# Optimization experiments

Hardware: AMD Instinct MI355X
Metric: run time of the kernel (lower is better)

## Reference

```python
import jax, jax.numpy as jnp
import numpy as np
from jax import lax

D_MODEL, D_STATE, D_CONV, D_INNER, DT_RANK = 1024, 16, 4, 2048, 64
B_SZ, L_SEQ = 2, 4096

def setup_inputs() -> dict:
    key = jax.random.key(0)
    ks = jax.random.split(key, 12)
    s = 0.02
    x = jax.random.normal(ks[0], (B_SZ, L_SEQ, D_MODEL), jnp.float32)
    norm_w = jnp.ones((D_MODEL,), jnp.float32)
    norm_b = jnp.zeros((D_MODEL,), jnp.float32)
    W_in = jax.random.normal(ks[1], (D_MODEL, 2 * D_INNER), jnp.float32) * s
    conv_w = jax.random.normal(ks[2], (D_INNER, 1, D_CONV), jnp.float32) * 0.5
    conv_b = jnp.zeros((D_INNER,), jnp.float32)
    W_x = jax.random.normal(ks[3], (D_INNER, DT_RANK + 2 * D_STATE), jnp.float32) * s
    W_dt = jax.random.normal(ks[4], (DT_RANK, D_INNER), jnp.float32) * s
    # dt bias init as in the torch module: inverse-softplus of dt in [dt_min, dt_max]
    dt_init = jnp.exp(jax.random.uniform(ks[5], (D_INNER,)) * (np.log(0.1) - np.log(0.001)) + np.log(0.001))
    dt_init = jnp.clip(dt_init, 1e-4, None)
    b_dt = dt_init + jnp.log(-jnp.expm1(-dt_init))
    A_log = jnp.log(jnp.broadcast_to(jnp.arange(1, D_STATE + 1, dtype=jnp.float32)[None, :], (D_INNER, D_STATE)))
    D = jnp.ones((D_INNER,), jnp.float32)
    W_out = jax.random.normal(ks[6], (D_INNER, D_MODEL), jnp.float32) * s
    return {"x": x, "norm_w": norm_w, "norm_b": norm_b, "W_in": W_in,
            "conv_w": conv_w, "conv_b": conv_b, "W_x": W_x, "W_dt": W_dt,
            "b_dt": b_dt, "A_log": A_log, "D": D, "W_out": W_out}

def _silu(v):
    return v * jax.nn.sigmoid(v)

def _layernorm(v, w, b, eps=1e-5):
    mu = jnp.mean(v, axis=-1, keepdims=True)
    var = jnp.var(v, axis=-1, keepdims=True)
    return (v - mu) * lax.rsqrt(var + eps) * w + b

def _selective_scan(u, delta, A, Bm, Cm, Dp):
    # u, delta: [B,L,d_inner]; A: [d_inner,N]; Bm, Cm: [B,L,N]; Dp: [d_inner]
    Bb, L, d_inner = u.shape
    N = A.shape[1]

    def step(h, inp):
        dt_t, u_t, B_t, C_t = inp  # [B,d_inner],[B,d_inner],[B,N],[B,N]
        A_bar = jnp.exp(dt_t[..., None] * A)                       # [B,d_inner,N]
        h = A_bar * h + dt_t[..., None] * B_t[:, None, :] * u_t[..., None]
        y = jnp.sum(h * C_t[:, None, :], axis=-1)                  # [B,d_inner]
        return h, y

    h0 = jnp.zeros((Bb, d_inner, N), u.dtype)
    xs = (jnp.swapaxes(delta, 0, 1), jnp.swapaxes(u, 0, 1),
          jnp.swapaxes(Bm, 0, 1), jnp.swapaxes(Cm, 0, 1))
    _, ys = lax.scan(step, h0, xs)          # ys: [L,B,d_inner]
    y = jnp.swapaxes(ys, 0, 1)
    return y + u * Dp[None, None, :]

def reference(x, norm_w, norm_b, W_in, conv_w, conv_b, W_x, W_dt, b_dt, A_log, D, W_out):
    residual = x
    xn = _layernorm(x, norm_w, norm_b)
    xz = xn @ W_in                                      # [B,L,2*d_inner]
    x_ssm, z = jnp.split(xz, 2, axis=-1)
    # depthwise causal conv1d (torch pads both sides then truncates -> left pad)
    xt = jnp.swapaxes(x_ssm, 1, 2)                      # [B,d_inner,L]
    xt = jnp.pad(xt, ((0, 0), (0, 0), (D_CONV - 1, 0)))
    xc = lax.conv_general_dilated(xt, conv_w, window_strides=(1,), padding='VALID',
                                  feature_group_count=D_INNER,
                                  dimension_numbers=('NCH', 'OIH', 'NCH'))
    xc = xc + conv_b[None, :, None]
    x_conv = jnp.swapaxes(_silu(xc), 1, 2)              # [B,L,d_inner]
    x_dbl = x_conv @ W_x                                # [B,L,dt_rank+2N]
    dt_low, B_mat, C_mat = jnp.split(x_dbl, [DT_RANK, DT_RANK + D_STATE], axis=-1)
    delta = jax.nn.softplus(dt_low @ W_dt + b_dt)       # [B,L,d_inner]
    A = -jnp.exp(A_log)
    y = _selective_scan(x_conv, delta, A, B_mat, C_mat, D)
    y = y * _silu(z)
    return residual + y @ W_out
```

## Files before the change

kernel.cpp:

```cpp
#include <hip/hip_runtime.h>

typedef unsigned short u16;
typedef __attribute__((ext_vector_type(8))) __bf16 bf16x8;
typedef __attribute__((ext_vector_type(4))) float f32x4;

#define LSEQ 4096
#define DMODEL 1024
#define DINNER 2048

__device__ __forceinline__ float bf2f(u16 u) {
  union { unsigned u; float f; } v; v.u = ((unsigned)u) << 16; return v.f;
}
__device__ __forceinline__ u16 f2bf(float f) {
  union { float f; unsigned u; } v; v.f = f;
  unsigned r = v.u + 0x7fffu + ((v.u >> 16) & 1u);
  return (u16)(r >> 16);
}
__device__ __forceinline__ void gload_lds16(const void* g, void* l) {
  __builtin_amdgcn_global_load_lds(
      (__attribute__((address_space(1))) void*)(unsigned long long)g,
      (__attribute__((address_space(3))) void*)(unsigned int)(unsigned long long)l,
      16, 0, 0);
}
__device__ __forceinline__ float sigmoidf_(float v) { return 1.f / (1.f + __expf(-v)); }

__device__ __forceinline__ void swz_block(int gx, int& bn, int& bm) {
  int lin = blockIdx.x + gridDim.x * blockIdx.y;
  int q = (gridDim.x * gridDim.y) >> 3;
  int s = (lin & 7) * q + (lin >> 3);
  bn = s % gx;
  bm = s / gx;
}

#define SBAR { __builtin_amdgcn_s_barrier(); __builtin_amdgcn_sched_barrier(0); }

__global__ __launch_bounds__(256) void tc_ln_all(const float* __restrict__ W_in,
                                                 const float* __restrict__ W_x,
                                                 const float* __restrict__ W_dt,
                                                 const float* __restrict__ W_out,
                                                 u16* __restrict__ o0, u16* __restrict__ o1,
                                                 u16* __restrict__ o2, u16* __restrict__ o3,
                                                 const float* __restrict__ x,
                                                 const float* __restrict__ nw,
                                                 const float* __restrict__ nb,
                                                 u16* __restrict__ xn_out) {
  int id = blockIdx.x;
  int t = threadIdx.x;
  if (id >= 6528) {
    int row = id - 6528;
    const float* xr = x + (size_t)row * DMODEL;
    float4 v = ((const float4*)xr)[t];
    float s = v.x + v.y + v.z + v.w;
    float s2 = v.x * v.x + v.y * v.y + v.z * v.z + v.w * v.w;
    for (int off = 32; off; off >>= 1) {
      s += __shfl_down(s, off);
      s2 += __shfl_down(s2, off);
    }
    __shared__ float ls[4], ls2[4];
    int wid = t >> 6;
    if ((t & 63) == 0) { ls[wid] = s; ls2[wid] = s2; }
    __syncthreads();
    s = ls[0] + ls[1] + ls[2] + ls[3];
    s2 = ls2[0] + ls2[1] + ls2[2] + ls2[3];
    float mu = s * (1.f / DMODEL);
    float var = s2 * (1.f / DMODEL) - mu * mu;
    float rs = rsqrtf(var + 1e-5f);
    float4 wv = ((const float4*)nw)[t];
    float4 bv = ((const float4*)nb)[t];
    unsigned p0 = (unsigned)f2bf((v.x - mu) * rs * wv.x + bv.x) |
                  ((unsigned)f2bf((v.y - mu) * rs * wv.y + bv.y) << 16);
    unsigned p1 = (unsigned)f2bf((v.z - mu) * rs * wv.z + bv.z) |
                  ((unsigned)f2bf((v.w - mu) * rs * wv.w + bv.w) << 16);
    ((uint2*)(xn_out + (size_t)row * DMODEL))[t] = make_uint2(p0, p1);
    return;
  }
  __shared__ float tile[32][33];
  const float* in;
  u16* out;
  int K, N, Npad, gx, bx;
  if (id < 4096)      { in = W_in;  out = o0; K = 1024; N = 4096; Npad = 4096; gx = 128; bx = id; }
  else if (id < 4352) { in = W_x;   out = o1; K = 2048; N = 96;   Npad = 128;  gx = 4;   bx = id - 4096; }
  else if (id < 4480) { in = W_dt;  out = o2; K = 64;   N = 2048; Npad = 2048; gx = 64;  bx = id - 4352; }
  else                { in = W_out; out = o3; K = 2048; N = 1024; Npad = 1024; gx = 32;  bx = id - 4480; }
  int n0 = (bx % gx) * 32, k0 = (bx / gx) * 32;
  int tx = t & 31, ty = t >> 5;
  for (int i = ty; i < 32; i += 8) {
    int k = k0 + i, n = n0 + tx;
    tile[i][tx] = (k < K && n < N) ? in[(size_t)k * N + n] : 0.f;
  }
  __syncthreads();
  for (int i = ty; i < 32; i += 8) {
    int n = n0 + i, k = k0 + tx;
    if (n < Npad && k < K) out[(size_t)n * K + k] = f2bf(tile[tx][i]);
  }
}

__device__ __forceinline__ void stage8(const u16* grow0, int ld, int kcol0,
                                       u16* lds_u, int ln) {
  int rr = ln >> 3, kb = ln & 7;
  gload_lds16(grow0 + (size_t)rr * ld + kcol0 + ((kb ^ rr) << 3), lds_u);
}

#define LDA_F(mh, BUF)                                                             \
  _Pragma("unroll") for (int mf = 0; mf < 4; ++mf) {                               \
    av[mf][0] = *(const bf16x8*)(qA0 + (BUF) * 16384 + ((mh) * 64 + mf * 16) * 64); \
    av[mf][1] = *(const bf16x8*)(qA1 + (BUF) * 16384 + ((mh) * 64 + mf * 16) * 64); \
  }

#define LDB_F(nh, BUF)                                                             \
  _Pragma("unroll") for (int nf = 0; nf < 2; ++nf) {                               \
    bb[nh][nf][0] = *(const bf16x8*)(qB0 + (BUF) * 16384 + ((nh) * 32 + nf * 16) * 64); \
    bb[nh][nf][1] = *(const bf16x8*)(qB1 + (BUF) * 16384 + ((nh) * 32 + nf * 16) * 64); \
  }

#define MFMA_Q(mh, nh)                                                             \
  __builtin_amdgcn_s_setprio(1);                                                   \
  _Pragma("unroll") for (int mf = 0; mf < 4; ++mf)                                 \
  _Pragma("unroll") for (int nf = 0; nf < 2; ++nf)                                 \
  _Pragma("unroll") for (int kk = 0; kk < 2; ++kk)                                 \
    acc[(mh) * 4 + mf][(nh) * 2 + nf] = __builtin_amdgcn_mfma_f32_16x16x32_bf16(   \
        av[mf][kk], bb[nh][nf][kk], acc[(mh) * 4 + mf][(nh) * 2 + nf], 0, 0, 0);   \
  __builtin_amdgcn_s_setprio(0);

#define STAGE_A(unit, kt, buf)                                                     \
  _Pragma("unroll") for (int c = 0; c < 2; ++c) {                                  \
    int g = w * 2 + c;                                                             \
    int r0 = ((g < 8) ? g * 8 : (g - 8) * 8 + 128) + (unit) * 64;                  \
    stage8(Ag + (size_t)r0 * ldK, ldK, (kt) * 64, LA + (buf) * 16384 + r0 * 64, ln); \
  }

#define STAGE_B(half, kt, buf)                                                     \
  _Pragma("unroll") for (int c = 0; c < 2; ++c) {                                  \
    int g = w * 2 + c;                                                             \
    int r0 = (g >> 2) * 64 + (half) * 32 + (g & 3) * 8;                            \
    stage8(Bg + (size_t)r0 * ldK, ldK, (kt) * 64, LB + (buf) * 16384 + r0 * 64, ln); \
  }

#define PHASES8P(T_, B0_, B1_)                                                     \
  {                                                                                \
    int kt1 = ((T_) + 1 < NT) ? (T_) + 1 : NT - 1;                                 \
    int kt2 = ((T_) + 2 < NT) ? (T_) + 2 : NT - 1;                                 \
    LDA_F(0, B0_); LDB_F(0, B0_); LDB_F(1, B0_);                                   \
    STAGE_A(1, kt1, B1_);                                                          \
    MFMA_Q(0, 0);                                                                  \
    MFMA_Q(0, 1);                                                                  \
    SBAR                                                                           \
    LDA_F(1, B0_);                                                                 \
    STAGE_A(0, kt2, B0_);                                                          \
    STAGE_B(0, kt2, B0_);                                                          \
    STAGE_B(1, kt2, B0_);                                                          \
    asm volatile("s_waitcnt vmcnt(6)" ::: "memory");                               \
    MFMA_Q(1, 1);                                                                  \
    MFMA_Q(1, 0);                                                                  \
    SBAR                                                                           \
  }

template <int OUT_BF16, int EPI>
__global__ __launch_bounds__(512, 2) void gemm8p(const u16* __restrict__ A,
                                                 const u16* __restrict__ Bt,
                                                 void* __restrict__ Cout,
                                                 const float* __restrict__ aux,
                                                 int M, int N, int K, int cthresh) {
  __shared__ alignas(16) u16 lds[65536];
  u16* LA = lds;
  u16* LB = lds + 32768;
  int t = threadIdx.x;
  int w = t >> 6, ln = t & 63;
  int wm = w >> 2, wn = w & 3;
  int bn, bm;
  swz_block(gridDim.x, bn, bm);
  int lr = ln & 15, lq = ln >> 4, key = ln & 7;
  int ldK = K;
  int NT = K >> 6;
  const u16* Ag = A + (size_t)bm * 256 * ldK;
  const u16* Bg = Bt + (size_t)bn * 256 * ldK;
  const u16* qA0 = LA + (wm * 128 + lr) * 64 + ((lq ^ key) << 3);
  const u16* qA1 = LA + (wm * 128 + lr) * 64 + (((4 + lq) ^ key) << 3);
  const u16* qB0 = LB + (wn * 64 + lr) * 64 + ((lq ^ key) << 3);
  const u16* qB1 = LB + (wn * 64 + lr) * 64 + (((4 + lq) ^ key) << 3);
  f32x4 acc[8][4] = {};
  bf16x8 av[4][2], bb[2][2][2];

  STAGE_A(0, 0, 0); STAGE_B(0, 0, 0); STAGE_B(1, 0, 0); STAGE_A(1, 0, 0);
  int k1 = NT > 1 ? 1 : 0;
  STAGE_A(0, k1, 1); STAGE_B(0, k1, 1); STAGE_B(1, k1, 1);
  asm volatile("s_waitcnt vmcnt(6)" ::: "memory");
  SBAR

  for (int TT = 0; TT < NT; TT += 2) {
    PHASES8P(TT, 0, 1)
    PHASES8P(TT + 1, 1, 0)
  }

  int crow0 = bm * 256 + wm * 128;
  int ccol0 = bn * 256 + wn * 64;
#pragma unroll
  for (int mf = 0; mf < 8; ++mf)
#pragma unroll
    for (int nf = 0; nf < 4; ++nf)
#pragma unroll
      for (int r = 0; r < 4; ++r) {
        int row = crow0 + mf * 16 + lq * 4 + r;
        int col = ccol0 + nf * 16 + lr;
        float v = acc[mf][nf][r];
        if (EPI == 1) v += aux[(size_t)row * N + col];
        if (EPI == 2 && col >= cthresh) v = v * sigmoidf_(v);
        if (OUT_BF16)
          ((u16*)Cout)[(size_t)row * N + col] = f2bf(v);
        else
          ((float*)Cout)[(size_t)row * N + col] = v;
      }
}

#define LDA128(mh, BUF)                                                            \
  _Pragma("unroll") for (int mf2 = 0; mf2 < 2; ++mf2) {                            \
    av[mf2][0] = *(const bf16x8*)(rA0 + (BUF) * 8192 + ((mh) * 32 + mf2 * 16) * 64); \
    av[mf2][1] = *(const bf16x8*)(rA1 + (BUF) * 8192 + ((mh) * 32 + mf2 * 16) * 64); \
  }

#define LDB128(nh, BUF, B_)                                                        \
  _Pragma("unroll") for (int nf2 = 0; nf2 < 2; ++nf2) {                            \
    B_[nf2][0] = *(const bf16x8*)(rB0 + (BUF) * 16384 + ((nh) * 32 + nf2 * 16) * 64); \
    B_[nf2][1] = *(const bf16x8*)(rB1 + (BUF) * 16384 + ((nh) * 32 + nf2 * 16) * 64); \
  }

#define MFMA_Q128(mh, nh, B_)                                                      \
  __builtin_amdgcn_s_setprio(1);                                                   \
  _Pragma("unroll") for (int mf2 = 0; mf2 < 2; ++mf2)                              \
  _Pragma("unroll") for (int nf2 = 0; nf2 < 2; ++nf2)                              \
  _Pragma("unroll") for (int kk = 0; kk < 2; ++kk)                                 \
    acc[(mh) * 2 + mf2][(nh) * 2 + nf2] = __builtin_amdgcn_mfma_f32_16x16x32_bf16( \
        av[mf2][kk], B_[nf2][kk], acc[(mh) * 2 + mf2][(nh) * 2 + nf2], 0, 0, 0);   \
  __builtin_amdgcn_s_setprio(0);

#define STAGE_A128(unit, kt, buf)                                                  \
  {                                                                                \
    int r0 = (w >> 2) * 64 + (unit) * 32 + (w & 3) * 8;                            \
    stage8(Ag + (size_t)r0 * ldK, ldK, (kt) * 64, LA + (buf) * 8192 + r0 * 64, ln); \
  }

#define STAGE_B128(half, kt, buf)                                                  \
  _Pragma("unroll") for (int c = 0; c < 2; ++c) {                                  \
    int g = w * 2 + c;                                                             \
    int r0 = (g >> 2) * 64 + (half) * 32 + (g & 3) * 8;                            \
    stage8(Bg + (size_t)r0 * ldK, ldK, (kt) * 64, LB + (buf) * 16384 + r0 * 64, ln); \
  }

#define PHASES128(T_, B0_, B1_)                                                    \
  {                                                                                \
    int kt1 = ((T_) + 1 < NT) ? (T_) + 1 : NT - 1;                                 \
    int kt2 = ((T_) + 2 < NT) ? (T_) + 2 : NT - 1;                                 \
    LDA128(0, B0_);                                                                \
    LDB128(0, B0_, bbl);                                                           \
    LDB128(1, B0_, bbh);                                                           \
    STAGE_A128(1, kt1, B1_);                                                       \
    MFMA_Q128(0, 0, bbl);                                                          \
    MFMA_Q128(0, 1, bbh);                                                          \
    SBAR                                                                           \
    LDA128(1, B0_);                                                                \
    STAGE_A128(0, kt2, B0_);                                                       \
    STAGE_B128(0, kt2, B0_);                                                       \
    STAGE_B128(1, kt2, B0_);                                                       \
    asm volatile("s_waitcnt vmcnt(5)" ::: "memory");                               \
    MFMA_Q128(1, 1, bbh);                                                          \
    MFMA_Q128(1, 0, bbl);                                                          \
    SBAR                                                                           \
  }

__global__ __launch_bounds__(512, 2) void gemm128_res(const u16* __restrict__ A,
                                                      const u16* __restrict__ Bt,
                                                      float* __restrict__ Cout,
                                                      const float* __restrict__ res,
                                                      int M, int N, int K) {
  __shared__ alignas(16) u16 lds[49152];
  u16* LA = lds;
  u16* LB = lds + 16384;
  int t = threadIdx.x;
  int w = t >> 6, ln = t & 63;
  int wm = w >> 2, wn = w & 3;
  int bn, bm;
  swz_block(gridDim.x, bn, bm);
  int lr = ln & 15, lq = ln >> 4, key = ln & 7;
  int ldK = K;
  int NT = K >> 6;
  const u16* Ag = A + (size_t)bm * 128 * ldK;
  const u16* Bg = Bt + (size_t)bn * 256 * ldK;
  const u16* rA0 = LA + (wm * 64 + lr) * 64 + ((lq ^ key) << 3);
  const u16* rA1 = LA + (wm * 64 + lr) * 64 + (((4 + lq) ^ key) << 3);
  const u16* rB0 = LB + (wn * 64 + lr) * 64 + ((lq ^ key) << 3);
  const u16* rB1 = LB + (wn * 64 + lr) * 64 + (((4 + lq) ^ key) << 3);
  f32x4 acc[4][4] = {};
  bf16x8 av[2][2], bbl[2][2], bbh[2][2];

  STAGE_A128(0, 0, 0); STAGE_B128(0, 0, 0); STAGE_B128(1, 0, 0); STAGE_A128(1, 0, 0);
  int k1 = NT > 1 ? 1 : 0;
  STAGE_A128(0, k1, 1); STAGE_B128(0, k1, 1); STAGE_B128(1, k1, 1);
  asm volatile("s_waitcnt vmcnt(5)" ::: "memory");
  SBAR

  for (int TT = 0; TT < NT; TT += 2) {
    PHASES128(TT, 0, 1)
    PHASES128(TT + 1, 1, 0)
  }

  int crow0 = bm * 128 + wm * 64;
  int ccol0 = bn * 256 + wn * 64;
#pragma unroll
  for (int mf = 0; mf < 4; ++mf)
#pragma unroll
    for (int nf = 0; nf < 4; ++nf)
#pragma unroll
      for (int r = 0; r < 4; ++r) {
        int row = crow0 + mf * 16 + lq * 4 + r;
        int col = ccol0 + nf * 16 + lr;
        Cout[(size_t)row * N + col] = acc[mf][nf][r] + res[(size_t)row * N + col];
      }
}

template <int OUT_BF16, int EPI, int SPLITK>
__global__ __launch_bounds__(256) void gemm_bt(const u16* __restrict__ A,
                                               const u16* __restrict__ Bt,
                                               void* __restrict__ Cout,
                                               const float* __restrict__ aux,
                                               int M, int N, int K, int ld, int cthresh) {
  __shared__ alignas(16) u16 As[128 * 32];
  __shared__ alignas(16) u16 Bs[128 * 32];
  int t = threadIdx.x;
  int w = t >> 6, ln = t & 63;
  int wr = w >> 1, wc = w & 1;
  int bm = blockIdx.y, bn = blockIdx.x;
  int lr = ln & 15, lk = (ln >> 4) * 8;
  f32x4 acc[4][4] = {};
  int kz = SPLITK ? blockIdx.z * K : 0;
  const u16* Abase = A + (size_t)bm * 128 * ld + kz;
  const u16* Bbase = Bt + (size_t)bn * 128 * ld + kz;
  for (int k0 = 0; k0 < K; k0 += 32) {
#pragma unroll
    for (int c = 0; c < 2; ++c) {
      int chunk = w * 2 + c;
      int ee = chunk * 512 + ln * 8;
      int row = ee >> 5, col = ee & 31;
      gload_lds16(Abase + (size_t)row * ld + k0 + col, As + chunk * 512);
      gload_lds16(Bbase + (size_t)row * ld + k0 + col, Bs + chunk * 512);
    }
    __syncthreads();
    bf16x8 af[4], bfr[4];
#pragma unroll
    for (int m = 0; m < 4; ++m)
      af[m] = *(const bf16x8*)(As + (wr * 64 + m * 16 + lr) * 32 + lk);
#pragma unroll
    for (int n = 0; n < 4; ++n)
      bfr[n] = *(const bf16x8*)(Bs + (wc * 64 + n * 16 + lr) * 32 + lk);
#pragma unroll
    for (int m = 0; m < 4; ++m)
#pragma unroll
      for (int n = 0; n < 4; ++n)
        acc[m][n] = __builtin_amdgcn_mfma_f32_16x16x32_bf16(af[m], bfr[n], acc[m][n], 0, 0, 0);
    __syncthreads();
  }
  int rb = bm * 128 + wr * 64 + (ln >> 4) * 4;
  int cb = bn * 128 + wc * 64 + lr;
  float* Cpart = SPLITK ? ((float*)Cout + (size_t)blockIdx.z * M * N) : (float*)Cout;
#pragma unroll
  for (int m = 0; m < 4; ++m)
#pragma unroll
    for (int n = 0; n < 4; ++n)
#pragma unroll
      for (int r = 0; r < 4; ++r) {
        int row = rb + m * 16 + r;
        int col = cb + n * 16;
        float v = acc[m][n][r];
        if (EPI == 3) {
          float dtr = v + aux[col];
          v = dtr > 15.f ? dtr : __logf(1.f + __expf(dtr));
        }
        if (OUT_BF16)
          ((u16*)Cpart)[(size_t)row * N + col] = f2bf(v);
        else
          Cpart[(size_t)row * N + col] = v;
      }
}

__global__ __launch_bounds__(256) void reduce_xdbl(const float* __restrict__ part,
                                                   float* __restrict__ xdbl,
                                                   u16* __restrict__ dtlow) {
  int i = blockIdx.x * 256 + threadIdx.x;
  float s = 0.f;
#pragma unroll
  for (int z = 0; z < 8; ++z) s += part[(size_t)z * (8192 * 128) + i];
  xdbl[i] = s;
  int col = i & 127;
  if (col < 64) dtlow[(size_t)(i >> 7) * 64 + col] = f2bf(s);
}

__global__ __launch_bounds__(256) void conv_silu(const u16* __restrict__ xz,
                                                 const float* __restrict__ cw,
                                                 const float* __restrict__ cb,
                                                 u16* __restrict__ out) {
  int d2 = blockIdx.x * 256 + threadIdx.x;
  int d = d2 * 2;
  int l0 = blockIdx.y * 8;
  int b = blockIdx.z;
  float w0a = cw[d * 4 + 0], w1a = cw[d * 4 + 1], w2a = cw[d * 4 + 2], w3a = cw[d * 4 + 3];
  float w0b = cw[d * 4 + 4], w1b = cw[d * 4 + 5], w2b = cw[d * 4 + 6], w3b = cw[d * 4 + 7];
  float biasa = cb[d], biasb = cb[d + 1];
  const u16* xp = xz + ((size_t)b * LSEQ) * 4096 + d;
  float xa[11], xb[11];
#pragma unroll
  for (int i = 0; i < 11; ++i) {
    int l = l0 - 3 + i;
    unsigned pk = (l >= 0) ? *(const unsigned*)(xp + (size_t)l * 4096) : 0u;
    xa[i] = bf2f((u16)(pk & 0xffffu));
    xb[i] = bf2f((u16)(pk >> 16));
  }
  u16* op = out + ((size_t)b * LSEQ + l0) * DINNER + d;
#pragma unroll
  for (int i = 0; i < 8; ++i) {
    float va = biasa + w0a * xa[i] + w1a * xa[i + 1] + w2a * xa[i + 2] + w3a * xa[i + 3];
    float vb = biasb + w0b * xb[i] + w1b * xb[i + 1] + w2b * xb[i + 2] + w3b * xb[i + 3];
    unsigned pk = (unsigned)f2bf(va * sigmoidf_(va)) |
                  ((unsigned)f2bf(vb * sigmoidf_(vb)) << 16);
    *(unsigned*)(op + (size_t)i * DINNER) = pk;
  }
}

__device__ __forceinline__ void compute_a(float dt, const float* An, bool fast, float* av) {
  if (fast) {
    float q = __expf(-dt);
    float q2 = q * q, q4 = q2 * q2;
    av[0] = q; av[1] = q2; av[2] = q2 * q; av[3] = q4;
#pragma unroll
    for (int n = 4; n < 16; ++n) av[n] = av[n - 4] * q4;
  } else {
#pragma unroll
    for (int n = 0; n < 16; ++n) av[n] = __expf(dt * An[n]);
  }
}

__device__ __forceinline__ void load_An(const float* A_log, int d, float* An, bool& fast) {
  const float4* A4 = (const float4*)(A_log + (size_t)d * 16);
  fast = true;
#pragma unroll
  for (int q = 0; q < 4; ++q) {
    float4 a = A4[q];
    An[q * 4 + 0] = -__expf(a.x);
    An[q * 4 + 1] = -__expf(a.y);
    An[q * 4 + 2] = -__expf(a.z);
    An[q * 4 + 3] = -__expf(a.w);
  }
#pragma unroll
  for (int n = 0; n < 16; ++n)
    fast = fast && (__builtin_fabsf(An[n] + (float)(n + 1)) < 1e-3f * (n + 1));
}

__global__ __launch_bounds__(256) void scan1(const u16* __restrict__ dtbf,
                                             const u16* __restrict__ ubf,
                                             const float* __restrict__ xdbl,
                                             const float* __restrict__ A_log,
                                             float* __restrict__ P,
                                             float* __restrict__ H) {
  int d = blockIdx.x * 256 + threadIdx.x;
  int b = blockIdx.y, c = blockIdx.z;
  size_t row0 = (size_t)b * LSEQ + c * 64;
  float An[16];
  bool fast;
  load_An(A_log, d, An, fast);
  const u16* dtp = dtbf + row0 * DINNER + d;
  const u16* up = ubf + row0 * DINNER + d;
  const float* Bp = xdbl + row0 * 128 + 64;
  float h[16];
#pragma unroll
  for (int n = 0; n < 16; ++n) h[n] = 0.f;
  float sdt = 0.f;
  float dt_c = bf2f(dtp[0]);
  float uu_c = bf2f(up[0]);
  const float4* B4 = (const float4*)Bp;
  float4 b0c = B4[0], b1c = B4[1], b2c = B4[2], b3c = B4[3];
  for (int i = 0; i < 64; ++i) {
    float dt_n = dt_c, uu_n = uu_c;
    float4 b0n = b0c, b1n = b1c, b2n = b2c, b3n = b3c;
    if (i < 63) {
      dt_n = bf2f(dtp[(size_t)(i + 1) * DINNER]);
      uu_n = bf2f(up[(size_t)(i + 1) * DINNER]);
      const float4* B4n = (const float4*)(Bp + (size_t)(i + 1) * 128);
      b0n = B4n[0]; b1n = B4n[1]; b2n = B4n[2]; b3n = B4n[3];
    }
    float dtu = dt_c * uu_c;
    sdt += dt_c;
    float Bf[16] = {b0c.x, b0c.y, b0c.z, b0c.w, b1c.x, b1c.y, b1c.z, b1c.w,
                    b2c.x, b2c.y, b2c.z, b2c.w, b3c.x, b3c.y, b3c.z, b3c.w};
    float av[16];
    compute_a(dt_c, An, fast, av);
#pragma unroll
    for (int n = 0; n < 16; ++n) h[n] = av[n] * h[n] + dtu * Bf[n];
    dt_c = dt_n; uu_c = uu_n;
    b0c = b0n; b1c = b1n; b2c = b2n; b3c = b3n;
  }
  size_t idx = (size_t)c * 65536 + ((size_t)b * DINNER + d) * 16;
  float4* P4 = (float4*)(P + idx);
  float4* H4 = (float4*)(H + idx);
#pragma unroll
  for (int q = 0; q < 4; ++q) {
    P4[q] = make_float4(__expf(An[q * 4 + 0] * sdt), __expf(An[q * 4 + 1] * sdt),
                        __expf(An[q * 4 + 2] * sdt), __expf(An[q * 4 + 3] * sdt));
    H4[q] = make_float4(h[q * 4], h[q * 4 + 1], h[q * 4 + 2], h[q * 4 + 3]);
  }
}

__global__ __launch_bounds__(256) void scan2(const float* __restrict__ P,
                                             const float* __restrict__ H,
                                             float* __restrict__ Hinit) {
  int i = blockIdx.x * 256 + threadIdx.x;
  float h = 0.f;
  for (int c = 0; c < 64; ++c) {
    Hinit[(size_t)c * 65536 + i] = h;
    h = P[(size_t)c * 65536 + i] * h + H[(size_t)c * 65536 + i];
  }
}

__global__ __launch_bounds__(256) void scan3(const u16* __restrict__ dtbf,
                                             const u16* __restrict__ ubf,
                                             const float* __restrict__ xdbl,
                                             const float* __restrict__ A_log,
                                             const float* __restrict__ Dp,
                                             const u16* __restrict__ xzbf,
                                             const float* __restrict__ Hinit,
                                             u16* __restrict__ ybf) {
  int d = blockIdx.x * 256 + threadIdx.x;
  int b = blockIdx.y, c = blockIdx.z;
  size_t row0 = (size_t)b * LSEQ + c * 64;
  float An[16];
  bool fast;
  load_An(A_log, d, An, fast);
  const u16* dtp = dtbf + row0 * DINNER + d;
  const u16* up = ubf + row0 * DINNER + d;
  const float* Bp = xdbl + row0 * 128 + 64;
  const float* Cp = xdbl + row0 * 128 + 80;
  const u16* gp = xzbf + row0 * 4096 + DINNER + d;
  u16* yp = ybf + row0 * DINNER + d;
  float Dv = Dp[d];
  float h[16];
  {
    const float4* Hi4 = (const float4*)(Hinit + (size_t)c * 65536 + ((size_t)b * DINNER + d) * 16);
#pragma unroll
    for (int q = 0; q < 4; ++q) {
      float4 hv = Hi4[q];
      h[q * 4 + 0] = hv.x; h[q * 4 + 1] = hv.y; h[q * 4 + 2] = hv.z; h[q * 4 + 3] = hv.w;
    }
  }
  float dt_c = bf2f(dtp[0]);
  float uu_c = bf2f(up[0]);
  float g_c = bf2f(gp[0]);
  const float4* B4 = (const float4*)Bp;
  const float4* C4 = (const float4*)Cp;
  float4 b0c = B4[0], b1c = B4[1], b2c = B4[2], b3c = B4[3];
  float4 c0c = C4[0], c1c = C4[1], c2c = C4[2], c3c = C4[3];
  for (int i = 0; i < 64; ++i) {
    float dt_n = dt_c, uu_n = uu_c, g_n = g_c;
    float4 b0n = b0c, b1n = b1c, b2n = b2c, b3n = b3c;
    float4 c0n = c0c, c1n = c1c, c2n = c2c, c3n = c3c;
    if (i < 63) {
      dt_n = bf2f(dtp[(size_t)(i + 1) * DINNER]);
      uu_n = bf2f(up[(size_t)(i + 1) * DINNER]);
      g_n = bf2f(gp[(size_t)(i + 1) * 4096]);
      const float4* B4n = (const float4*)(Bp + (size_t)(i + 1) * 128);
      const float4* C4n = (const float4*)(Cp + (size_t)(i + 1) * 128);
      b0n = B4n[0]; b1n = B4n[1]; b2n = B4n[2]; b3n = B4n[3];
      c0n = C4n[0]; c1n = C4n[1]; c2n = C4n[2]; c3n = C4n[3];
    }
    float dtu = dt_c * uu_c;
    float Bf[16] = {b0c.x, b0c.y, b0c.z, b0c.w, b1c.x, b1c.y, b1c.z, b1c.w,
                    b2c.x, b2c.y, b2c.z, b2c.w, b3c.x, b3c.y, b3c.z, b3c.w};
    float Cf[16] = {c0c.x, c0c.y, c0c.z, c0c.w, c1c.x, c1c.y, c1c.z, c1c.w,
                    c2c.x, c2c.y, c2c.z, c2c.w, c3c.x, c3c.y, c3c.z, c3c.w};
    float av[16];
    compute_a(dt_c, An, fast, av);
    float y = 0.f;
#pragma unroll
    for (int n = 0; n < 16; ++n) {
      h[n] = av[n] * h[n] + dtu * Bf[n];
      y += h[n] * Cf[n];
    }
    yp[(size_t)i * DINNER] = f2bf((y + uu_c * Dv) * g_c);
    dt_c = dt_n; uu_c = uu_n; g_c = g_n;
    b0c = b0n; b1c = b1n; b2c = b2n; b3c = b3n;
    c0c = c0n; c1c = c1n; c2c = c2n; c3c = c3n;
  }
}

extern "C" void kernel_launch(void* const* d_in, const int* in_sizes, int n_in,
                              void* d_out, int out_size, void* d_ws, size_t ws_size,
                              hipStream_t stream) {
  const float* x = (const float*)d_in[0];
  const float* nw = (const float*)d_in[1];
  const float* nb = (const float*)d_in[2];
  const float* W_in = (const float*)d_in[3];
  const float* convw = (const float*)d_in[4];
  const float* convb = (const float*)d_in[5];
  const float* W_x = (const float*)d_in[6];
  const float* W_dt = (const float*)d_in[7];
  const float* b_dt = (const float*)d_in[8];
  const float* A_log = (const float*)d_in[9];
  const float* Dp = (const float*)d_in[10];
  const float* W_out = (const float*)d_in[11];
  float* out = (float*)d_out;

  char* wp = (char*)d_ws;
  auto alloc = [&](size_t bytes) {
    char* p = wp;
    wp += (bytes + 255) & ~(size_t)255;
    return p;
  };
  u16* xz_bf = (u16*)alloc((size_t)8192 * 4096 * 2);
  u16* xconv_bf = (u16*)alloc((size_t)8192 * 2048 * 2);
  u16* xn_bf = (u16*)alloc((size_t)8192 * 1024 * 2);
  float* xdbl = (float*)alloc((size_t)8192 * 128 * 4);
  u16* dt_bf = (u16*)alloc((size_t)8192 * 2048 * 2);
  u16* dtlow_bf = (u16*)alloc((size_t)8192 * 64 * 2);
  u16* Wint = (u16*)alloc((size_t)4096 * 1024 * 2);
  u16* Wxt = (u16*)alloc((size_t)128 * 2048 * 2);
  u16* Wdtt = (u16*)alloc((size_t)2048 * 64 * 2);
  u16* Woutt = (u16*)alloc((size_t)1024 * 2048 * 2);
  float* P = (float*)alloc((size_t)64 * 65536 * 4);
  float* H = (float*)alloc((size_t)64 * 65536 * 4);
  float* Hinit = (float*)alloc((size_t)64 * 65536 * 4);
  float* xdbl_part = (float*)P;
  u16* y_bf = (u16*)P;

  tc_ln_all<<<6528 + 8192, 256, 0, stream>>>(W_in, W_x, W_dt, W_out, Wint, Wxt, Wdtt, Woutt,
                                             x, nw, nb, xn_bf);

  gemm8p<1, 2><<<dim3(16, 32), 512, 0, stream>>>(xn_bf, Wint, xz_bf, nullptr,
                                                 8192, 4096, 1024, 2048);
  conv_silu<<<dim3(4, 512, 2), 256, 0, stream>>>(xz_bf, convw, convb, xconv_bf);
  gemm_bt<0, 0, 1><<<dim3(1, 64, 8), 256, 0, stream>>>(xconv_bf, Wxt, xdbl_part, nullptr,
                                                       8192, 128, 256, 2048, 0);
  reduce_xdbl<<<4096, 256, 0, stream>>>(xdbl_part, xdbl, dtlow_bf);
  gemm_bt<1, 3, 0><<<dim3(16, 64), 256, 0, stream>>>(dtlow_bf, Wdtt, dt_bf, b_dt,
                                                     8192, 2048, 64, 64, 0);
  scan1<<<dim3(8, 2, 64), 256, 0, stream>>>(dt_bf, xconv_bf, xdbl, A_log, P, H);
  scan2<<<256, 256, 0, stream>>>(P, H, Hinit);
  scan3<<<dim3(8, 2, 64), 256, 0, stream>>>(dt_bf, xconv_bf, xdbl, A_log, Dp, xz_bf,
                                            Hinit, y_bf);
  gemm128_res<<<dim3(4, 64), 512, 0, stream>>>(y_bf, Woutt, out, x, 8192, 1024, 2048);
}
```

Baseline: 306.1 us.

## Store chunk scan states in bf16 and recompute decay products from summed dt

The chunked scan now writes per-chunk end states and initial states as bf16 instead of fp32. It also replaces the per-state decay product tensor P with a single per-channel dt sum, and scan2 recomputes exp(A*sdt) from that sum. This cuts the traffic between scan1, scan2 and scan3 roughly in half or more, in exchange for extra exp work in scan2 and lower precision in the carried states. Scan2 stays a serial 64-chunk loop over only 256 blocks, so its latency is only partly reduced.

```diff
diff --git a/kernel.cpp b/kernel.cpp
--- a/kernel.cpp
+++ b/kernel.cpp
@@ -457,8 +457,8 @@
                                              const u16* __restrict__ ubf,
                                              const float* __restrict__ xdbl,
                                              const float* __restrict__ A_log,
-                                             float* __restrict__ P,
-                                             float* __restrict__ H) {
+                                             float* __restrict__ sdt_out,
+                                             u16* __restrict__ H_bf) {
   int d = blockIdx.x * 256 + threadIdx.x;
   int b = blockIdx.y, c = blockIdx.z;
   size_t row0 = (size_t)b * LSEQ + c * 64;
@@ -496,25 +496,30 @@
     dt_c = dt_n; uu_c = uu_n;
     b0c = b0n; b1c = b1n; b2c = b2n; b3c = b3n;
   }
-  size_t idx = (size_t)c * 65536 + ((size_t)b * DINNER + d) * 16;
-  float4* P4 = (float4*)(P + idx);
-  float4* H4 = (float4*)(H + idx);
-#pragma unroll
-  for (int q = 0; q < 4; ++q) {
-    P4[q] = make_float4(__expf(An[q * 4 + 0] * sdt), __expf(An[q * 4 + 1] * sdt),
-                        __expf(An[q * 4 + 2] * sdt), __expf(An[q * 4 + 3] * sdt));
-    H4[q] = make_float4(h[q * 4], h[q * 4 + 1], h[q * 4 + 2], h[q * 4 + 3]);
-  }
-}
-
-__global__ __launch_bounds__(256) void scan2(const float* __restrict__ P,
-                                             const float* __restrict__ H,
-                                             float* __restrict__ Hinit) {
+  int bd = b * DINNER + d;
+  sdt_out[(size_t)c * 4096 + bd] = sdt;
+  unsigned wds[8];
+#pragma unroll
+  for (int q = 0; q < 8; ++q)
+    wds[q] = (unsigned)f2bf(h[2 * q]) | ((unsigned)f2bf(h[2 * q + 1]) << 16);
+  uint4* Hp = (uint4*)(H_bf + (size_t)c * 65536 + (size_t)bd * 16);
+  Hp[0] = make_uint4(wds[0], wds[1], wds[2], wds[3]);
+  Hp[1] = make_uint4(wds[4], wds[5], wds[6], wds[7]);
+}
+
+__global__ __launch_bounds__(256) void scan2(const u16* __restrict__ H_bf,
+                                             const float* __restrict__ sdt,
+                                             const float* __restrict__ A_log,
+                                             u16* __restrict__ Hinit_bf) {
   int i = blockIdx.x * 256 + threadIdx.x;
+  int n = i & 15, bd = i >> 4;
+  int d = bd & 2047;
+  float An = -__expf(A_log[d * 16 + n]);
   float h = 0.f;
   for (int c = 0; c < 64; ++c) {
-    Hinit[(size_t)c * 65536 + i] = h;
-    h = P[(size_t)c * 65536 + i] * h + H[(size_t)c * 65536 + i];
+    Hinit_bf[(size_t)c * 65536 + i] = f2bf(h);
+    float p = __expf(An * sdt[(size_t)c * 4096 + bd]);
+    h = p * h + bf2f(H_bf[(size_t)c * 65536 + i]);
   }
 }
 
@@ -524,7 +529,7 @@
                                              const float* __restrict__ A_log,
                                              const float* __restrict__ Dp,
                                              const u16* __restrict__ xzbf,
-                                             const float* __restrict__ Hinit,
+                                             const u16* __restrict__ Hinit_bf,
                                              u16* __restrict__ ybf) {
   int d = blockIdx.x * 256 + threadIdx.x;
   int b = blockIdx.y, c = blockIdx.z;
@@ -541,11 +546,14 @@
   float Dv = Dp[d];
   float h[16];
   {
-    const float4* Hi4 = (const float4*)(Hinit + (size_t)c * 65536 + ((size_t)b * DINNER + d) * 16);
-#pragma unroll
-    for (int q = 0; q < 4; ++q) {
-      float4 hv = Hi4[q];
-      h[q * 4 + 0] = hv.x; h[q * 4 + 1] = hv.y; h[q * 4 + 2] = hv.z; h[q * 4 + 3] = hv.w;
+    const uint4* Hi4 = (const uint4*)(Hinit_bf + (size_t)c * 65536 +
+                                      ((size_t)b * DINNER + d) * 16);
+    uint4 p0 = Hi4[0], p1 = Hi4[1];
+    unsigned wd[8] = {p0.x, p0.y, p0.z, p0.w, p1.x, p1.y, p1.z, p1.w};
+#pragma unroll
+    for (int q = 0; q < 8; ++q) {
+      h[2 * q] = bf2f((u16)(wd[q] & 0xffffu));
+      h[2 * q + 1] = bf2f((u16)(wd[q] >> 16));
     }
   }
   float dt_c = bf2f(dtp[0]);
@@ -625,6 +633,9 @@
   float* H = (float*)alloc((size_t)64 * 65536 * 4);
   float* Hinit = (float*)alloc((size_t)64 * 65536 * 4);
   float* xdbl_part = (float*)P;
+  float* sdtP = (float*)P;
+  u16* H_bf16 = (u16*)H;
+  u16* Hinit_bf16 = (u16*)Hinit;
   u16* y_bf = (u16*)P;
 
   tc_ln_all<<<6528 + 8192, 256, 0, stream>>>(W_in, W_x, W_dt, W_out, Wint, Wxt, Wdtt, Woutt,
@@ -638,9 +649,9 @@
   reduce_xdbl<<<4096, 256, 0, stream>>>(xdbl_part, xdbl, dtlow_bf);
   gemm_bt<1, 3, 0><<<dim3(16, 64), 256, 0, stream>>>(dtlow_bf, Wdtt, dt_bf, b_dt,
                                                      8192, 2048, 64, 64, 0);
-  scan1<<<dim3(8, 2, 64), 256, 0, stream>>>(dt_bf, xconv_bf, xdbl, A_log, P, H);
-  scan2<<<256, 256, 0, stream>>>(P, H, Hinit);
+  scan1<<<dim3(8, 2, 64), 256, 0, stream>>>(dt_bf, xconv_bf, xdbl, A_log, sdtP, H_bf16);
+  scan2<<<256, 256, 0, stream>>>(H_bf16, sdtP, A_log, Hinit_bf16);
   scan3<<<dim3(8, 2, 64), 256, 0, stream>>>(dt_bf, xconv_bf, xdbl, A_log, Dp, xz_bf,
-                                            Hinit, y_bf);
+                                            Hinit_bf16, y_bf);
   gemm128_res<<<dim3(4, 64), 512, 0, stream>>>(y_bf, Woutt, out, x, 8192, 1024, 2048);
 }
```

Measured after the change: 307.3 us, median of 2. Within noise of the previous version (+0.4%).
